# Performance work log

Hardware: AMD Instinct MI355X
Metric: run time of the kernel (lower is better)

Reference implementation:

```python
import jax, jax.numpy as jnp
import numpy as np

BATCH_SIZE = 4096
DIM = 512
TEMPERATURE = 0.5
NUM_CLASSES = 100
EPS = 1e-8  # torch CosineSimilarity eps


def setup_inputs() -> dict:
    key = jax.random.key(0)
    k1, k2, k3 = jax.random.split(key, 3)
    z = jax.random.normal(k1, (BATCH_SIZE, DIM), dtype=jnp.float32)
    z_adv = jax.random.normal(k2, (BATCH_SIZE, DIM), dtype=jnp.float32)
    labels = jax.random.randint(k3, (BATCH_SIZE,), 0, NUM_CLASSES, dtype=jnp.int64)
    return {"z": z, "z_adv": z_adv, "labels": labels}


def _normalize(x):
    # torch.nn.CosineSimilarity clamps norm at eps
    n = jnp.sqrt(jnp.sum(x * x, axis=-1, keepdims=True))
    return x / jnp.maximum(n, EPS)


def reference(z, z_adv, labels):
    N = z.shape[0]
    zn = _normalize(z)            # [N, D]
    zan = _normalize(z_adv)       # [N, D]
    # per-sample clean-vs-adv cosine similarity
    sim_adv = jnp.sum(zn * zan, axis=1) / TEMPERATURE      # [N]
    sim_adv_e = jnp.exp(sim_adv)
    # pairwise cosine similarity via normalize + matmul (same math as
    # the broadcasted CosineSimilarity(dim=2) in the original)
    sim = jnp.einsum('nd,md->nm', zn, zn) / TEMPERATURE     # [N, N]
    # mask: same label, off-diagonal
    same = labels[None, :] == labels[:, None]
    mask = same & ~jnp.eye(N, dtype=bool)
    intra = jnp.sum(jnp.exp(sim) * mask.astype(sim.dtype), axis=1)  # [N]
    loss = -jnp.log(sim_adv_e / (sim_adv_e + intra))
    return jnp.sum(loss) / N
```

## Files before the change

kernel.cpp:

```cpp
#include <hip/hip_runtime.h>
#include <math.h>

#define N      4096
#define DIM    512
#define NCLS   100
#define INV_T  2.0f
#define EPSN   1e-8f
#define CAP    96
#define NTMAX  (CAP / 16)
#define FRAG_SHORTS (NTMAX * 16 * 64 * 8)
#define SMEM_BYTES (FRAG_SHORTS * 2 + CAP * 4 + 8 * 4)

typedef __attribute__((ext_vector_type(8))) short short8;
typedef __attribute__((ext_vector_type(4))) float float4v;

__device__ __forceinline__ float dot8(const float4& a0, const float4& a1,
                                      const float4& b0, const float4& b1) {
    float p = a0.x * b0.x;
    p = fmaf(a0.y, b0.y, p); p = fmaf(a0.z, b0.z, p); p = fmaf(a0.w, b0.w, p);
    p = fmaf(a1.x, b1.x, p); p = fmaf(a1.y, b1.y, p);
    p = fmaf(a1.z, b1.z, p); p = fmaf(a1.w, b1.w, p);
    return p;
}

__device__ __forceinline__ short f2bf(float x) {
    unsigned u = __float_as_uint(x);
    unsigned r = (u + 0x7FFFu + ((u >> 16) & 1u)) >> 16;
    return (short)r;
}

__global__ void rownorm_kernel(const float* __restrict__ z,
                               const float* __restrict__ za,
                               const int*   __restrict__ labels,
                               float* __restrict__ norms,
                               float* __restrict__ simadv,
                               int*   __restrict__ counts,
                               int*   __restrict__ bucket) {
    const int wave = threadIdx.x >> 6, lane = threadIdx.x & 63;
    const int i = blockIdx.x * 4 + wave;
    const float4* zi4 = (const float4*)(z  + (size_t)i * DIM);
    const float4* ai4 = (const float4*)(za + (size_t)i * DIM);
    float4 z0 = zi4[lane * 2], z1 = zi4[lane * 2 + 1];
    float4 a0 = ai4[lane * 2], a1 = ai4[lane * 2 + 1];
    float zz  = dot8(z0, z1, z0, z1);
    float aa  = dot8(a0, a1, a0, a1);
    float zad = dot8(z0, z1, a0, a1);
    #pragma unroll
    for (int off = 32; off >= 1; off >>= 1) {
        zz  += __shfl_xor(zz,  off);
        aa  += __shfl_xor(aa,  off);
        zad += __shfl_xor(zad, off);
    }
    if (lane == 0) {
        float nz = fmaxf(sqrtf(zz), EPSN);
        float na = fmaxf(sqrtf(aa), EPSN);
        norms[i]  = nz;
        simadv[i] = zad / (nz * na) * INV_T;
        int lab = labels[i];
        int pos = atomicAdd(&counts[lab], 1);
        if (pos < CAP) bucket[lab * CAP + pos] = i;
    }
}

__global__ __launch_bounds__(256, 1)
void loss_kernel(const float* __restrict__ z,
                 const float* __restrict__ norms,
                 const float* __restrict__ simadv,
                 const int*   __restrict__ counts,
                 const int*   __restrict__ bucket,
                 float* __restrict__ out) {
    extern __shared__ char smem[];
    short* frag  = (short*)smem;
    float* intra = (float*)(smem + FRAG_SHORTS * 2);
    float* wred  = (float*)(smem + FRAG_SHORTS * 2 + CAP * 4);

    const int c    = blockIdx.x;
    const int tid  = threadIdx.x;
    const int wave = tid >> 6, lane = tid & 63;
    int m = counts[c]; if (m > CAP) m = CAP;
    const int nt   = (m + 15) >> 4;
    const int base = c * CAP;

    const int kt_w = lane >> 2, q_w = lane & 3;
    for (int s = wave; s < nt * 16; s += 4) {
        const int tile = s >> 4, col = s & 15;
        short8 v;
        if (s < m) {
            const int j = bucket[base + s];
            const float rn = 1.0f / norms[j];
            const float4* zr = (const float4*)(z + (size_t)j * DIM);
            float4 f0 = zr[lane * 2], f1 = zr[lane * 2 + 1];
            v[0] = f2bf(f0.x * rn); v[1] = f2bf(f0.y * rn);
            v[2] = f2bf(f0.z * rn); v[3] = f2bf(f0.w * rn);
            v[4] = f2bf(f1.x * rn); v[5] = f2bf(f1.y * rn);
            v[6] = f2bf(f1.z * rn); v[7] = f2bf(f1.w * rn);
        } else {
            v = (short8)0;
        }
        *(short8*)(frag + (((size_t)(tile * 16 + kt_w) * 64 + q_w * 16 + col) * 8)) = v;
    }
    __syncthreads();

    const int q = lane >> 4, col = lane & 15;
    for (int ti = wave; ti < nt; ti += 4) {
        short8 a[16];
        #pragma unroll
        for (int kt = 0; kt < 16; ++kt)
            a[kt] = *(const short8*)(frag + (((ti * 16 + kt) * 64 + lane) * 8));
        float racc0 = 0.f, racc1 = 0.f, racc2 = 0.f, racc3 = 0.f;
        const int irow = ti * 16 + q * 4;
        for (int tj = 0; tj < nt; ++tj) {
            float4v acc = {0.f, 0.f, 0.f, 0.f};
            #pragma unroll
            for (int kt = 0; kt < 16; ++kt) {
                short8 b = *(const short8*)(frag + (((tj * 16 + kt) * 64 + lane) * 8));
                acc = __builtin_amdgcn_mfma_f32_16x16x32_bf16(a[kt], b, acc, 0, 0, 0);
            }
            const int jslot = tj * 16 + col;
            const bool jok = (jslot < m);
            racc0 += (jok && (irow + 0) != jslot) ? __expf(acc[0] * INV_T) : 0.f;
            racc1 += (jok && (irow + 1) != jslot) ? __expf(acc[1] * INV_T) : 0.f;
            racc2 += (jok && (irow + 2) != jslot) ? __expf(acc[2] * INV_T) : 0.f;
            racc3 += (jok && (irow + 3) != jslot) ? __expf(acc[3] * INV_T) : 0.f;
        }
        #pragma unroll
        for (int off = 1; off < 16; off <<= 1) {
            racc0 += __shfl_xor(racc0, off);
            racc1 += __shfl_xor(racc1, off);
            racc2 += __shfl_xor(racc2, off);
            racc3 += __shfl_xor(racc3, off);
        }
        if (col == 0) {
            intra[irow + 0] = racc0;
            intra[irow + 1] = racc1;
            intra[irow + 2] = racc2;
            intra[irow + 3] = racc3;
        }
    }
    __syncthreads();

    float lsum = 0.f;
    for (int s = tid; s < m; s += 256) {
        const int i = bucket[base + s];
        const float sa = simadv[i];
        lsum += logf(__expf(sa) + intra[s]) - sa;
    }
    #pragma unroll
    for (int off = 32; off >= 1; off >>= 1) lsum += __shfl_xor(lsum, off);
    if (lane == 0) wred[wave] = lsum;
    __syncthreads();
    if (tid == 0)
        atomicAdd(out, (wred[0] + wred[1] + wred[2] + wred[3]) * (1.0f / (float)N));
}

extern "C" void kernel_launch(void* const* d_in, const int* in_sizes, int n_in,
                              void* d_out, int out_size, void* d_ws, size_t ws_size,
                              hipStream_t stream) {
    const float* z      = (const float*)d_in[0];
    const float* z_adv  = (const float*)d_in[1];
    const int*   labels = (const int*)d_in[2];

    char* ws = (char*)d_ws;
    float* norms   = (float*)(ws);
    float* simadv  = (float*)(ws + 16384);
    int*   counts  = (int*)  (ws + 32768);
    int*   bucket  = (int*)  (ws + 33280);

    static int attr_done = 0;
    if (!attr_done) {
        hipFuncSetAttribute((const void*)loss_kernel,
                            hipFuncAttributeMaxDynamicSharedMemorySize, SMEM_BYTES);
        attr_done = 1;
    }

    hipMemsetAsync(counts, 0, NCLS * sizeof(int), stream);
    hipMemsetAsync(d_out, 0, sizeof(float), stream);

    rownorm_kernel<<<N / 4, 256, 0, stream>>>(z, z_adv, labels, norms, simadv,
                                              counts, bucket);
    loss_kernel   <<<NCLS, 256, SMEM_BYTES, stream>>>(z, norms, simadv, counts,
                                                      bucket, (float*)d_out);
}
```

Baseline: 93.16 us.

## Fuse row-norm and per-class loss into a single kernel with in-block bucketing

Merges the row-norm/bucketing kernel into the per-class loss kernel. Each block scans all labels to build its own member list in shared memory, then computes norms and adversarial similarity for its rows while packing the bf16 fragments. This removes one kernel launch, a memset and the global workspace round trip. In exchange, each of the 100 blocks rereads the full label array and the row-norm work now runs on only 100 blocks instead of 1024.

```diff
diff --git a/kernel.cpp b/kernel.cpp
--- a/kernel.cpp
+++ b/kernel.cpp
@@ -9,7 +9,13 @@
 #define CAP    96
 #define NTMAX  (CAP / 16)
 #define FRAG_SHORTS (NTMAX * 16 * 64 * 8)
-#define SMEM_BYTES (FRAG_SHORTS * 2 + CAP * 4 + 8 * 4)
+
+#define OFF_INTRA (FRAG_SHORTS * 2)
+#define OFF_SADV  (OFF_INTRA + CAP * 4)
+#define OFF_SLOT  (OFF_SADV  + CAP * 4)
+#define OFF_WRED  (OFF_SLOT  + CAP * 4)
+#define OFF_CNT   (OFF_WRED  + 4 * 4)
+#define SMEM_BYTES (OFF_CNT + 4)
 
 typedef __attribute__((ext_vector_type(8))) short short8;
 typedef __attribute__((ext_vector_type(4))) float float4v;
@@ -29,67 +35,58 @@
     return (short)r;
 }
 
-__global__ void rownorm_kernel(const float* __restrict__ z,
-                               const float* __restrict__ za,
-                               const int*   __restrict__ labels,
-                               float* __restrict__ norms,
-                               float* __restrict__ simadv,
-                               int*   __restrict__ counts,
-                               int*   __restrict__ bucket) {
-    const int wave = threadIdx.x >> 6, lane = threadIdx.x & 63;
-    const int i = blockIdx.x * 4 + wave;
-    const float4* zi4 = (const float4*)(z  + (size_t)i * DIM);
-    const float4* ai4 = (const float4*)(za + (size_t)i * DIM);
-    float4 z0 = zi4[lane * 2], z1 = zi4[lane * 2 + 1];
-    float4 a0 = ai4[lane * 2], a1 = ai4[lane * 2 + 1];
-    float zz  = dot8(z0, z1, z0, z1);
-    float aa  = dot8(a0, a1, a0, a1);
-    float zad = dot8(z0, z1, a0, a1);
-    #pragma unroll
-    for (int off = 32; off >= 1; off >>= 1) {
-        zz  += __shfl_xor(zz,  off);
-        aa  += __shfl_xor(aa,  off);
-        zad += __shfl_xor(zad, off);
-    }
-    if (lane == 0) {
-        float nz = fmaxf(sqrtf(zz), EPSN);
-        float na = fmaxf(sqrtf(aa), EPSN);
-        norms[i]  = nz;
-        simadv[i] = zad / (nz * na) * INV_T;
-        int lab = labels[i];
-        int pos = atomicAdd(&counts[lab], 1);
-        if (pos < CAP) bucket[lab * CAP + pos] = i;
-    }
-}
-
 __global__ __launch_bounds__(256, 1)
-void loss_kernel(const float* __restrict__ z,
-                 const float* __restrict__ norms,
-                 const float* __restrict__ simadv,
-                 const int*   __restrict__ counts,
-                 const int*   __restrict__ bucket,
-                 float* __restrict__ out) {
+void ial_fused_kernel(const float* __restrict__ z,
+                      const float* __restrict__ za,
+                      const int*   __restrict__ labels,
+                      float* __restrict__ out) {
     extern __shared__ char smem[];
     short* frag  = (short*)smem;
-    float* intra = (float*)(smem + FRAG_SHORTS * 2);
-    float* wred  = (float*)(smem + FRAG_SHORTS * 2 + CAP * 4);
+    float* intra = (float*)(smem + OFF_INTRA);
+    float* sadv  = (float*)(smem + OFF_SADV);
+    int*   slot  = (int*)  (smem + OFF_SLOT);
+    float* wred  = (float*)(smem + OFF_WRED);
+    int*   cnt   = (int*)  (smem + OFF_CNT);
 
     const int c    = blockIdx.x;
     const int tid  = threadIdx.x;
     const int wave = tid >> 6, lane = tid & 63;
-    int m = counts[c]; if (m > CAP) m = CAP;
-    const int nt   = (m + 15) >> 4;
-    const int base = c * CAP;
+
+    if (tid == 0) *cnt = 0;
+    __syncthreads();
+    for (int t = tid; t < N; t += 256) {
+        if (labels[t] == c) {
+            int p = atomicAdd(cnt, 1);
+            if (p < CAP) slot[p] = t;
+        }
+    }
+    __syncthreads();
+    int m = *cnt; if (m > CAP) m = CAP;
+    const int nt = (m + 15) >> 4;
 
     const int kt_w = lane >> 2, q_w = lane & 3;
     for (int s = wave; s < nt * 16; s += 4) {
         const int tile = s >> 4, col = s & 15;
         short8 v;
         if (s < m) {
-            const int j = bucket[base + s];
-            const float rn = 1.0f / norms[j];
-            const float4* zr = (const float4*)(z + (size_t)j * DIM);
+            const int j = slot[s];
+            const float4* zr = (const float4*)(z  + (size_t)j * DIM);
+            const float4* ar = (const float4*)(za + (size_t)j * DIM);
             float4 f0 = zr[lane * 2], f1 = zr[lane * 2 + 1];
+            float4 g0 = ar[lane * 2], g1 = ar[lane * 2 + 1];
+            float zz  = dot8(f0, f1, f0, f1);
+            float aa  = dot8(g0, g1, g0, g1);
+            float zad = dot8(f0, f1, g0, g1);
+            #pragma unroll
+            for (int off = 32; off >= 1; off >>= 1) {
+                zz  += __shfl_xor(zz,  off);
+                aa  += __shfl_xor(aa,  off);
+                zad += __shfl_xor(zad, off);
+            }
+            const float nz = fmaxf(sqrtf(zz), EPSN);
+            const float na = fmaxf(sqrtf(aa), EPSN);
+            const float rn = 1.0f / nz;
+            if (lane == 0) sadv[s] = zad / (nz * na) * INV_T;
             v[0] = f2bf(f0.x * rn); v[1] = f2bf(f0.y * rn);
             v[2] = f2bf(f0.z * rn); v[3] = f2bf(f0.w * rn);
             v[4] = f2bf(f1.x * rn); v[5] = f2bf(f1.y * rn);
@@ -141,8 +138,7 @@
 
     float lsum = 0.f;
     for (int s = tid; s < m; s += 256) {
-        const int i = bucket[base + s];
-        const float sa = simadv[i];
+        const float sa = sadv[s];
         lsum += logf(__expf(sa) + intra[s]) - sa;
     }
     #pragma unroll
@@ -160,24 +156,14 @@
     const float* z_adv  = (const float*)d_in[1];
     const int*   labels = (const int*)d_in[2];
 
-    char* ws = (char*)d_ws;
-    float* norms   = (float*)(ws);
-    float* simadv  = (float*)(ws + 16384);
-    int*   counts  = (int*)  (ws + 32768);
-    int*   bucket  = (int*)  (ws + 33280);
-
     static int attr_done = 0;
     if (!attr_done) {
-        hipFuncSetAttribute((const void*)loss_kernel,
+        hipFuncSetAttribute((const void*)ial_fused_kernel,
                             hipFuncAttributeMaxDynamicSharedMemorySize, SMEM_BYTES);
         attr_done = 1;
     }
 
-    hipMemsetAsync(counts, 0, NCLS * sizeof(int), stream);
     hipMemsetAsync(d_out, 0, sizeof(float), stream);
-
-    rownorm_kernel<<<N / 4, 256, 0, stream>>>(z, z_adv, labels, norms, simadv,
-                                              counts, bucket);
-    loss_kernel   <<<NCLS, 256, SMEM_BYTES, stream>>>(z, norms, simadv, counts,
-                                                      bucket, (float*)d_out);
+    ial_fused_kernel<<<NCLS, 256, SMEM_BYTES, stream>>>(z, z_adv, labels,
+                                                        (float*)d_out);
 }
```

Result: faster. 85.66 us (-8.0%).
